# Optimization experiments

Hardware: AMD Instinct MI355X
Metric: run time of the kernel (lower is better)

The kernel has to match this reference:

```python
import jax, jax.numpy as jnp
import numpy as np

N_NODES = 100000
N_EDGES = 1600000
N_GRAPHS = 64
IN_CH = 128
HID = 128
N_CLASSES = 8


def setup_inputs() -> dict:
    key = jax.random.key(0)
    ks = jax.random.split(key, 8)
    x = jax.random.normal(ks[0], (N_NODES, IN_CH), dtype=jnp.float32)
    edge_index = jax.random.randint(ks[1], (2, N_EDGES), 0, N_NODES, dtype=jnp.int64)
    batch = jnp.sort(jax.random.randint(ks[2], (N_NODES,), 0, N_GRAPHS, dtype=jnp.int64))
    s1 = 1.0 / np.sqrt(IN_CH)
    s2 = 1.0 / np.sqrt(HID)
    W1 = jax.random.normal(ks[3], (IN_CH, HID), dtype=jnp.float32) * s1
    b1 = jnp.zeros((HID,), dtype=jnp.float32)
    W2 = jax.random.normal(ks[4], (HID, HID), dtype=jnp.float32) * s2
    b2 = jnp.zeros((HID,), dtype=jnp.float32)
    lin_W = jax.random.normal(ks[5], (HID, N_CLASSES), dtype=jnp.float32) * s2
    lin_b = jnp.zeros((N_CLASSES,), dtype=jnp.float32)
    return {"x": x, "edge_index": edge_index, "batch": batch,
            "W1": W1, "b1": b1, "W2": W2, "b2": b2,
            "lin_W": lin_W, "lin_b": lin_b}


def _gcn_norm(edge_index, n_nodes):
    # add self-loops, compute symmetric normalization coefficients
    loops = jnp.arange(n_nodes, dtype=edge_index.dtype)
    src = jnp.concatenate([edge_index[0], loops])
    dst = jnp.concatenate([edge_index[1], loops])
    ones = jnp.ones(src.shape[0], dtype=jnp.float32)
    deg = jax.ops.segment_sum(ones, dst, num_segments=n_nodes)
    dinv = jnp.where(deg > 0, jax.lax.rsqrt(jnp.maximum(deg, 1.0)), 0.0)
    norm = dinv[src] * dinv[dst]  # [E + N]
    return src, dst, norm


def _gcn_conv(x, W, b, src, dst, norm, n_nodes):
    xw = x @ W                               # [N, H]
    msg = xw[src] * norm[:, None]            # gather + scale, [E+N, H]
    out = jax.ops.segment_sum(msg, dst, num_segments=n_nodes)
    return out + b


def reference(x, edge_index, batch, W1, b1, W2, b2, lin_W, lin_b):
    n = x.shape[0]
    src, dst, norm = _gcn_norm(edge_index, n)
    h = jax.nn.relu(_gcn_conv(x, W1, b1, src, dst, norm, n))
    h = _gcn_conv(h, W2, b2, src, dst, norm, n)
    # global mean pool over graphs
    sums = jax.ops.segment_sum(h, batch, num_segments=N_GRAPHS)
    cnts = jax.ops.segment_sum(jnp.ones(n, dtype=h.dtype), batch, num_segments=N_GRAPHS)
    pooled = sums / jnp.maximum(cnts, 1.0)[:, None]
    return pooled @ lin_W + lin_b
```

## Files before the change

### kernel.cpp

```cpp
#include <hip/hip_runtime.h>
#include <hip/hip_fp16.h>
#include <cstdint>
#include <cstddef>

#define NNODES 100000
#define NEDGES 1600000
#define NGRAPHS 64
#define BSHIFT 7
#define BRANGE 128
#define NB 782
#define CAP 4096
#define NZ NB
#define LP 136
#define NAB 25000

typedef short short8v __attribute__((ext_vector_type(8)));
typedef float float4v __attribute__((ext_vector_type(4)));

__device__ inline short f2h_s(float f) {
    __half h = __float2half(f);
    return __builtin_bit_cast(short, h);
}
__device__ inline ushort f2h_u(float f) {
    __half h = __float2half(f);
    return __builtin_bit_cast(ushort, h);
}
__device__ inline __half2 u2h2(uint u) { return __builtin_bit_cast(__half2, u); }
__device__ inline uint h22u(__half2 h) { return __builtin_bit_cast(uint, h); }


__global__ __launch_bounds__(256) void k_setup(int* __restrict__ zb,
                                               const float* __restrict__ W1,
                                               const float* __restrict__ W2,
                                               short8v* __restrict__ o1,
                                               short8v* __restrict__ o2,
                                               const int* __restrict__ batch,
                                               int* __restrict__ gstart,
                                               int* __restrict__ gend) {
    int b = blockIdx.x, t = threadIdx.x;
    if (b < 4) {
        int i = b * 256 + t;
        if (i < NZ) zb[i] = 0;
    } else if (b < 6) {
        const float* W = (b == 5) ? W2 : W1;
        short8v* o = (b == 5) ? o2 : o1;
        for (int s = t; s < 2048; s += 256) {
            int p = s >> 6, l = s & 63;
            int kb = (p >> 3) * 32 + ((l >> 4) * 8);
            int j = (p & 7) * 16 + (l & 15);
            short8v v;
            #pragma unroll
            for (int i = 0; i < 8; ++i)
                v[i] = f2h_s(W[(size_t)(kb + i) * 128 + j]);
            o[s] = v;
        }
    } else {
        int i = (b - 6) * 256 + t;
        if (i < NNODES) {
            int bb = batch[i];
            if (i == 0 || batch[i - 1] != bb) gstart[bb] = i;
            if (i == NNODES - 1 || batch[i + 1] != bb) gend[bb] = i + 1;
        }
    }
}


#define P1_EPT 16
__global__ __launch_bounds__(256) void k_bscatter(const int* __restrict__ src,
                                                  const int* __restrict__ dst,
                                                  int* __restrict__ bcur,
                                                  uint* __restrict__ pairs, int E) {
    __shared__ int h[NB];
    __shared__ int base[NB];
    int t = threadIdx.x;
    long long c0 = (long long)blockIdx.x * 4096;
    if (c0 >= E) return;
    for (int i = t; i < NB; i += 256) h[i] = 0;
    __syncthreads();
    int myb[P1_EPT], mylp[P1_EPT];
    uint myv[P1_EPT];
    #pragma unroll
    for (int k = 0; k < P1_EPT; ++k) {
        long long e = c0 + t + k * 256;
        if (e < E) {
            int d = dst[e];
            myv[k] = (uint)src[e] | ((uint)(d & (BRANGE - 1)) << 24);
            myb[k] = d >> BSHIFT;
            mylp[k] = atomicAdd(&h[myb[k]], 1);
        } else myb[k] = -1;
    }
    __syncthreads();
    for (int i = t; i < NB; i += 256)
        base[i] = h[i] ? atomicAdd(&bcur[i], h[i]) : 0;
    __syncthreads();
    #pragma unroll
    for (int k = 0; k < P1_EPT; ++k)
        if (myb[k] >= 0) {
            int pos = base[myb[k]] + mylp[k];
            if (pos < CAP)
                pairs[(size_t)myb[k] * CAP + pos] = myv[k];
        }
}


__global__ __launch_bounds__(256) void k_build(const uint* __restrict__ pairs,
                                               const int* __restrict__ bcur,
                                               int2* __restrict__ nr,
                                               float* __restrict__ dinv,
                                               int* __restrict__ csr, int N) {
    __shared__ int h[256];
    __shared__ int sh[256];
    __shared__ int cur[BRANGE];
    int b = blockIdx.x, t = threadIdx.x;
    h[t] = 0;
    __syncthreads();
    const int p0 = b * CAP;
    const int cntb = min(bcur[b], CAP);
    for (int p = t; p < cntb; p += 256)
        atomicAdd(&h[pairs[p0 + p] >> 24], 1);
    __syncthreads();
    int myh = h[t];
    sh[t] = myh;
    __syncthreads();
    #pragma unroll
    for (int d = 1; d < 256; d <<= 1) {
        int val = (t >= d) ? sh[t - d] : 0;
        __syncthreads();
        sh[t] += val;
        __syncthreads();
    }
    int excl = sh[t] - myh;
    int node = (b << BSHIFT) + t;
    if (t < BRANGE) {
        cur[t] = p0 + excl;
        if (node < N) {
            nr[node] = make_int2(p0 + excl, p0 + excl + myh);
            dinv[node] = rsqrtf((float)(myh + 1));
        }
    }
    __syncthreads();
    for (int p = t; p < cntb; p += 256) {
        uint pr = pairs[p0 + p];
        int pos = atomicAdd(&cur[pr >> 24], 1);
        csr[pos] = (int)(pr & 0x00FFFFFFu);
    }
}


__global__ __launch_bounds__(256) void k_gemm_f32(const float* __restrict__ X,
                                                  const short8v* __restrict__ wf,
                                                  const float* __restrict__ dinv,
                                                  ushort* __restrict__ Y, int nrows) {
    __shared__ short8v sW[2048];
    const int tid = threadIdx.x;
    const int lane = tid & 63;
    const int w = tid >> 6;

    for (int s = tid; s < 2048; s += 256) sW[s] = wf[s];
    __syncthreads();

    const int row0 = blockIdx.x * 64 + w * 16;
    const int arow = row0 + (lane & 15);
    float4v acc[8];
    #pragma unroll
    for (int ct = 0; ct < 8; ++ct) acc[ct] = (float4v)0.f;

    #pragma unroll
    for (int kk = 0; kk < 4; ++kk) {
        short8v a = (short8v)0;
        if (arow < nrows) {
            const float* xp = X + (size_t)arow * 128 + kk * 32 + ((lane >> 4) * 8);
            float4 f0 = ((const float4*)xp)[0];
            float4 f1 = ((const float4*)xp)[1];
            a[0] = f2h_s(f0.x); a[1] = f2h_s(f0.y);
            a[2] = f2h_s(f0.z); a[3] = f2h_s(f0.w);
            a[4] = f2h_s(f1.x); a[5] = f2h_s(f1.y);
            a[6] = f2h_s(f1.z); a[7] = f2h_s(f1.w);
        }
        #pragma unroll
        for (int ct = 0; ct < 8; ++ct)
            acc[ct] = __builtin_amdgcn_mfma_f32_16x16x32_f16(a, sW[(kk * 8 + ct) * 64 + lane],
                                                             acc[ct], 0, 0, 0);
    }

    const int orow = row0 + ((lane >> 4) << 2);
    #pragma unroll
    for (int r = 0; r < 4; ++r) {
        int row = orow + r;
        if (row < nrows) {
            float dr = dinv[row];
            #pragma unroll
            for (int ct = 0; ct < 8; ++ct)
                Y[(size_t)row * 128 + ct * 16 + (lane & 15)] = f2h_u(acc[ct][r] * dr);
        }
    }
}


__global__ __launch_bounds__(256, 8) void k_agg_gemm(const uint* __restrict__ msg,
                                                     const float* __restrict__ dinv,
                                                     const int2* __restrict__ nr,
                                                     const int* __restrict__ csr,
                                                     const float* __restrict__ bias,
                                                     const short8v* __restrict__ wf,
                                                     ushort* __restrict__ Y, int n) {
    __shared__ ushort ht[16 * LP];
    const int t = threadIdx.x;
    const int lane = t & 63;
    const int w = t >> 6;
    const int row0 = blockIdx.x * 16;
    const float bx = bias[lane * 2];
    const float by = bias[lane * 2 + 1];

    for (int i = 0; i < 4; ++i) {
        const int r = w * 4 + i;
        const int wid = row0 + r;
        __half2 a0 = u2h2(msg[(size_t)wid * 64 + lane]);
        __half2 a1 = u2h2(0u), a2 = u2h2(0u);
        const int2 rg = nr[wid];
        const int e0 = rg.x, e1 = rg.y;
        for (int e = e0; e < e1; e += 64) {
            int me = e + lane;
            int sidx = (me < e1) ? csr[me] : 0;
            int cnt = min(64, e1 - e);
            for (int kb = 0; kb < cnt; kb += 6) {
                int lim = cnt - 1;
                int s0 = __shfl(sidx, min(kb + 0, lim));
                int s1 = __shfl(sidx, min(kb + 1, lim));
                int s2 = __shfl(sidx, min(kb + 2, lim));
                int s3 = __shfl(sidx, min(kb + 3, lim));
                int s4 = __shfl(sidx, min(kb + 4, lim));
                int s5 = __shfl(sidx, min(kb + 5, lim));
                uint u0 = msg[(size_t)s0 * 64 + lane];
                uint u1 = msg[(size_t)s1 * 64 + lane];
                uint u2 = msg[(size_t)s2 * 64 + lane];
                uint u3 = msg[(size_t)s3 * 64 + lane];
                uint u4 = msg[(size_t)s4 * 64 + lane];
                uint u5 = msg[(size_t)s5 * 64 + lane];
                u1 = (kb + 1 < cnt) ? u1 : 0u;
                u2 = (kb + 2 < cnt) ? u2 : 0u;
                u3 = (kb + 3 < cnt) ? u3 : 0u;
                u4 = (kb + 4 < cnt) ? u4 : 0u;
                u5 = (kb + 5 < cnt) ? u5 : 0u;
                a0 = __hadd2(a0, u2h2(u0));
                a1 = __hadd2(a1, u2h2(u1));
                a2 = __hadd2(a2, u2h2(u2));
                a0 = __hadd2(a0, u2h2(u3));
                a1 = __hadd2(a1, u2h2(u4));
                a2 = __hadd2(a2, u2h2(u5));
            }
        }
        __half2 acc = __hadd2(__hadd2(a0, a1), a2);
        float2 f = __half22float2(acc);
        float dd = dinv[wid];
        float ax = fmaxf(f.x * dd + bx, 0.f);
        float ay = fmaxf(f.y * dd + by, 0.f);
        *(uint*)&ht[r * LP + lane * 2] = h22u(__floats2half2_rn(ax, ay));
    }
    __syncthreads();

    float4v acc[2];
    acc[0] = (float4v)0.f;
    acc[1] = (float4v)0.f;
    const int arow = lane & 15;
    const int ct0 = w * 2;
    #pragma unroll
    for (int kk = 0; kk < 4; ++kk) {
        short8v a = *(const short8v*)&ht[arow * LP + kk * 32 + ((lane >> 4) * 8)];
        acc[0] = __builtin_amdgcn_mfma_f32_16x16x32_f16(a, wf[(kk * 8 + ct0) * 64 + lane],
                                                        acc[0], 0, 0, 0);
        acc[1] = __builtin_amdgcn_mfma_f32_16x16x32_f16(a, wf[(kk * 8 + ct0 + 1) * 64 + lane],
                                                        acc[1], 0, 0, 0);
    }
    const int orow = row0 + ((lane >> 4) << 2);
    #pragma unroll
    for (int r = 0; r < 4; ++r) {
        int row = orow + r;
        float dr = dinv[row];
        Y[(size_t)row * 128 + ct0 * 16 + (lane & 15)]       = f2h_u(acc[0][r] * dr);
        Y[(size_t)row * 128 + (ct0 + 1) * 16 + (lane & 15)] = f2h_u(acc[1][r] * dr);
    }
}


__global__ __launch_bounds__(256) void k_agg_pool(const uint* __restrict__ msg,
                                                  const float* __restrict__ dinv,
                                                  const int2* __restrict__ nr,
                                                  const int* __restrict__ csr,
                                                  const int* __restrict__ batch,
                                                  float* __restrict__ pA,
                                                  float* __restrict__ pB) {
    __shared__ float red[4][128];
    __shared__ int selw[4];
    const int blk = blockIdx.x;
    const int t = threadIdx.x;
    const int lane = t & 63;
    const int w = t >> 6;
    const int wid = blk * 4 + w;

    __half2 a0 = u2h2(msg[(size_t)wid * 64 + lane]);
    __half2 a1 = u2h2(0u), a2 = u2h2(0u);
    const int2 rg = nr[wid];
    const int e0 = rg.x, e1 = rg.y;
    for (int e = e0; e < e1; e += 64) {
        int me = e + lane;
        int sidx = (me < e1) ? csr[me] : 0;
        int cnt = min(64, e1 - e);
        for (int kb = 0; kb < cnt; kb += 6) {
            int lim = cnt - 1;
            int s0 = __shfl(sidx, min(kb + 0, lim));
            int s1 = __shfl(sidx, min(kb + 1, lim));
            int s2 = __shfl(sidx, min(kb + 2, lim));
            int s3 = __shfl(sidx, min(kb + 3, lim));
            int s4 = __shfl(sidx, min(kb + 4, lim));
            int s5 = __shfl(sidx, min(kb + 5, lim));
            uint u0 = msg[(size_t)s0 * 64 + lane];
            uint u1 = msg[(size_t)s1 * 64 + lane];
            uint u2 = msg[(size_t)s2 * 64 + lane];
            uint u3 = msg[(size_t)s3 * 64 + lane];
            uint u4 = msg[(size_t)s4 * 64 + lane];
            uint u5 = msg[(size_t)s5 * 64 + lane];
            u1 = (kb + 1 < cnt) ? u1 : 0u;
            u2 = (kb + 2 < cnt) ? u2 : 0u;
            u3 = (kb + 3 < cnt) ? u3 : 0u;
            u4 = (kb + 4 < cnt) ? u4 : 0u;
            u5 = (kb + 5 < cnt) ? u5 : 0u;
            a0 = __hadd2(a0, u2h2(u0));
            a1 = __hadd2(a1, u2h2(u1));
            a2 = __hadd2(a2, u2h2(u2));
            a0 = __hadd2(a0, u2h2(u3));
            a1 = __hadd2(a1, u2h2(u4));
            a2 = __hadd2(a2, u2h2(u5));
        }
    }
    __half2 acc = __hadd2(__hadd2(a0, a1), a2);
    float2 f = __half22float2(acc);
    float dd = dinv[wid];
    red[w][lane * 2] = f.x * dd;
    red[w][lane * 2 + 1] = f.y * dd;
    if (lane == 0) selw[w] = (batch[wid] != batch[blk * 4]) ? 1 : 0;
    __syncthreads();
    if (t < 128) {
        float a = 0.f, b = 0.f;
        #pragma unroll
        for (int ww = 0; ww < 4; ++ww) {
            float v = red[ww][t];
            if (selw[ww]) b += v; else a += v;
        }
        pA[(size_t)blk * 128 + t] = a;
        if (selw[0] | selw[1] | selw[2] | selw[3])
            pB[(size_t)blk * 128 + t] = b;
    }
}


__global__ __launch_bounds__(512) void k_final(const float* __restrict__ pA,
                                               const float* __restrict__ pB,
                                               const int* __restrict__ batch,
                                               const int* __restrict__ gstart,
                                               const int* __restrict__ gend,
                                               const float* __restrict__ b2,
                                               const float* __restrict__ linW,
                                               const float* __restrict__ linb,
                                               float* __restrict__ out) {
    __shared__ float sq[4][128];
    __shared__ float red[128][8];
    int g = blockIdx.x;
    int t = threadIdx.x;
    int c = t & 127;
    int q = t >> 7;
    int b0 = gstart[g] >> 2;
    int b1 = (gend[g] - 1) >> 2;
    float v = 0.f;
    #pragma unroll 4
    for (int b = b0 + 1 + q; b <= b1; b += 4)
        v += pA[(size_t)b * 128 + c];
    if (q == 0)
        v += ((batch[b0 * 4] != g) ? pB : pA)[(size_t)b0 * 128 + c];
    sq[q][c] = v;
    __syncthreads();
    if (t < 128) {
        float sv = sq[0][t] + sq[1][t] + sq[2][t] + sq[3][t];
        float cnt = (float)(gend[g] - gstart[g]);
        sv = sv / fmaxf(cnt, 1.0f) + b2[t];
        #pragma unroll
        for (int k = 0; k < 8; ++k) red[t][k] = sv * linW[(size_t)t * 8 + k];
    }
    __syncthreads();
    #pragma unroll
    for (int st = 64; st > 0; st >>= 1) {
        if (t < st) {
            #pragma unroll
            for (int k = 0; k < 8; ++k) red[t][k] += red[t + st][k];
        }
        __syncthreads();
    }
    if (t < 8) out[(size_t)g * 8 + t] = red[0][t] + linb[t];
}


extern "C" void kernel_launch(void* const* d_in, const int* in_sizes, int n_in,
                              void* d_out, int out_size, void* d_ws, size_t ws_size,
                              hipStream_t stream) {
    const float* x     = (const float*)d_in[0];
    const int*   ei    = (const int*)d_in[1];
    const int*   batch = (const int*)d_in[2];
    const float* W1    = (const float*)d_in[3];
    const float* b1    = (const float*)d_in[4];
    const float* W2    = (const float*)d_in[5];
    const float* b2    = (const float*)d_in[6];
    const float* linW  = (const float*)d_in[7];
    const float* linb  = (const float*)d_in[8];
    float* out = (float*)d_out;

    const int N = NNODES, E = NEDGES;
    const int* src = ei;
    const int* dst = ei + E;

    char* ws = (char*)d_ws;
    uint*  bufA16 = (uint*)ws;     ws += (size_t)N * 64 * 4;
    uint*  bufH16 = (uint*)ws;     ws += (size_t)N * 64 * 4;
    float* dinv   = (float*)ws;    ws += (size_t)N * 4;
    int2*  nr     = (int2*)ws;     ws += (size_t)N * 8;
    int*   csr    = (int*)ws;      ws += (size_t)NB * CAP * 4;
    int*   bcur   = (int*)ws;      ws += NB * 4;
    int*   gstart = (int*)ws;      ws += NGRAPHS * 4;
    int*   gend   = (int*)ws;      ws += NGRAPHS * 4;
    short8v* wf1  = (short8v*)ws;  ws += 2048 * 16;
    short8v* wf2  = (short8v*)ws;  ws += 2048 * 16;
    float* pA     = (float*)ws;    ws += (size_t)NAB * 128 * 4;
    float* pB     = (float*)ws;    ws += (size_t)NAB * 128 * 4;
    uint*  pairs  = (uint*)bufH16;

    const int B = 256;

    k_setup<<<397, B, 0, stream>>>(bcur, W1, W2, wf1, wf2, batch, gstart, gend);

    k_bscatter<<<(E + 4095) / 4096, B, 0, stream>>>(src, dst, bcur, pairs, E);
    k_build<<<NB, B, 0, stream>>>(pairs, bcur, nr, dinv, csr, N);

    k_gemm_f32<<<(N + 63) / 64, B, 0, stream>>>(x, wf1, dinv, (ushort*)bufA16, N);

    k_agg_gemm<<<N / 16, B, 0, stream>>>(bufA16, dinv, nr, csr, b1, wf2,
                                         (ushort*)bufH16, N);

    k_agg_pool<<<NAB, B, 0, stream>>>(bufH16, dinv, nr, csr, batch, pA, pB);

    k_final<<<NGRAPHS, 512, 0, stream>>>(pA, pB, batch, gstart, gend, b2, linW, linb, out);
}
```

Before: 204.5 us.

## Stage X tiles through LDS in first GEMM and widen aggregation blocks

The first GEMM now handles 16 rows per block. It stages the fp32 rows as fp16 in shared memory with coalesced float4 loads and reads W fragments straight from global memory, so each block no longer copies the full 32KB weight into LDS. The aggregation+GEMM kernel moves to 512 threads, with 8 waves each aggregating 2 rows and computing one 16-column tile. This raises parallelism in the gather phase, at the cost of more blocks each reloading weights from global/L2 and dropping the nrows bounds check (N is divisible by 16).

```diff
diff --git a/kernel.cpp b/kernel.cpp
--- a/kernel.cpp
+++ b/kernel.cpp
@@ -147,63 +147,58 @@
 }
 
 
-__global__ __launch_bounds__(256) void k_gemm_f32(const float* __restrict__ X,
+__global__ __launch_bounds__(256) void k_gemm_f32(const float4* __restrict__ X4,
                                                   const short8v* __restrict__ wf,
                                                   const float* __restrict__ dinv,
-                                                  ushort* __restrict__ Y, int nrows) {
-    __shared__ short8v sW[2048];
-    const int tid = threadIdx.x;
-    const int lane = tid & 63;
-    const int w = tid >> 6;
-
-    for (int s = tid; s < 2048; s += 256) sW[s] = wf[s];
-    __syncthreads();
-
-    const int row0 = blockIdx.x * 64 + w * 16;
-    const int arow = row0 + (lane & 15);
-    float4v acc[8];
-    #pragma unroll
-    for (int ct = 0; ct < 8; ++ct) acc[ct] = (float4v)0.f;
-
+                                                  ushort* __restrict__ Y, int n) {
+    __shared__ ushort ht[16 * LP];
+    const int t = threadIdx.x;
+    const int lane = t & 63;
+    const int w = t >> 6;
+    const int row0 = blockIdx.x * 16;
+
+    #pragma unroll
+    for (int s = t; s < 16 * 32; s += 256) {
+        int row = s >> 5, q = s & 31;
+        float4 v = X4[(size_t)(row0 + row) * 32 + q];
+        ushort2 h0 = make_ushort2(f2h_u(v.x), f2h_u(v.y));
+        ushort2 h1 = make_ushort2(f2h_u(v.z), f2h_u(v.w));
+        *(ushort2*)&ht[row * LP + q * 4] = h0;
+        *(ushort2*)&ht[row * LP + q * 4 + 2] = h1;
+    }
+    __syncthreads();
+
+    float4v acc[2];
+    acc[0] = (float4v)0.f;
+    acc[1] = (float4v)0.f;
+    const int arow = lane & 15;
+    const int ct0 = w * 2;
     #pragma unroll
     for (int kk = 0; kk < 4; ++kk) {
-        short8v a = (short8v)0;
-        if (arow < nrows) {
-            const float* xp = X + (size_t)arow * 128 + kk * 32 + ((lane >> 4) * 8);
-            float4 f0 = ((const float4*)xp)[0];
-            float4 f1 = ((const float4*)xp)[1];
-            a[0] = f2h_s(f0.x); a[1] = f2h_s(f0.y);
-            a[2] = f2h_s(f0.z); a[3] = f2h_s(f0.w);
-            a[4] = f2h_s(f1.x); a[5] = f2h_s(f1.y);
-            a[6] = f2h_s(f1.z); a[7] = f2h_s(f1.w);
-        }
-        #pragma unroll
-        for (int ct = 0; ct < 8; ++ct)
-            acc[ct] = __builtin_amdgcn_mfma_f32_16x16x32_f16(a, sW[(kk * 8 + ct) * 64 + lane],
-                                                             acc[ct], 0, 0, 0);
-    }
-
+        short8v a = *(const short8v*)&ht[arow * LP + kk * 32 + ((lane >> 4) * 8)];
+        acc[0] = __builtin_amdgcn_mfma_f32_16x16x32_f16(a, wf[(kk * 8 + ct0) * 64 + lane],
+                                                        acc[0], 0, 0, 0);
+        acc[1] = __builtin_amdgcn_mfma_f32_16x16x32_f16(a, wf[(kk * 8 + ct0 + 1) * 64 + lane],
+                                                        acc[1], 0, 0, 0);
+    }
     const int orow = row0 + ((lane >> 4) << 2);
     #pragma unroll
     for (int r = 0; r < 4; ++r) {
         int row = orow + r;
-        if (row < nrows) {
-            float dr = dinv[row];
-            #pragma unroll
-            for (int ct = 0; ct < 8; ++ct)
-                Y[(size_t)row * 128 + ct * 16 + (lane & 15)] = f2h_u(acc[ct][r] * dr);
-        }
-    }
-}
-
-
-__global__ __launch_bounds__(256, 8) void k_agg_gemm(const uint* __restrict__ msg,
-                                                     const float* __restrict__ dinv,
-                                                     const int2* __restrict__ nr,
-                                                     const int* __restrict__ csr,
-                                                     const float* __restrict__ bias,
-                                                     const short8v* __restrict__ wf,
-                                                     ushort* __restrict__ Y, int n) {
+        float dr = dinv[row];
+        Y[(size_t)row * 128 + ct0 * 16 + (lane & 15)]       = f2h_u(acc[0][r] * dr);
+        Y[(size_t)row * 128 + (ct0 + 1) * 16 + (lane & 15)] = f2h_u(acc[1][r] * dr);
+    }
+}
+
+
+__global__ __launch_bounds__(512) void k_agg_gemm(const uint* __restrict__ msg,
+                                                  const float* __restrict__ dinv,
+                                                  const int2* __restrict__ nr,
+                                                  const int* __restrict__ csr,
+                                                  const float* __restrict__ bias,
+                                                  const short8v* __restrict__ wf,
+                                                  ushort* __restrict__ Y, int n) {
     __shared__ ushort ht[16 * LP];
     const int t = threadIdx.x;
     const int lane = t & 63;
@@ -212,8 +207,9 @@
     const float bx = bias[lane * 2];
     const float by = bias[lane * 2 + 1];
 
-    for (int i = 0; i < 4; ++i) {
-        const int r = w * 4 + i;
+    #pragma unroll
+    for (int i = 0; i < 2; ++i) {
+        const int r = w * 2 + i;
         const int wid = row0 + r;
         __half2 a0 = u2h2(msg[(size_t)wid * 64 + lane]);
         __half2 a1 = u2h2(0u), a2 = u2h2(0u);
@@ -259,26 +255,20 @@
     }
     __syncthreads();
 
-    float4v acc[2];
-    acc[0] = (float4v)0.f;
-    acc[1] = (float4v)0.f;
+    float4v acc = (float4v)0.f;
     const int arow = lane & 15;
-    const int ct0 = w * 2;
     #pragma unroll
     for (int kk = 0; kk < 4; ++kk) {
         short8v a = *(const short8v*)&ht[arow * LP + kk * 32 + ((lane >> 4) * 8)];
-        acc[0] = __builtin_amdgcn_mfma_f32_16x16x32_f16(a, wf[(kk * 8 + ct0) * 64 + lane],
-                                                        acc[0], 0, 0, 0);
-        acc[1] = __builtin_amdgcn_mfma_f32_16x16x32_f16(a, wf[(kk * 8 + ct0 + 1) * 64 + lane],
-                                                        acc[1], 0, 0, 0);
+        acc = __builtin_amdgcn_mfma_f32_16x16x32_f16(a, wf[(kk * 8 + w) * 64 + lane],
+                                                     acc, 0, 0, 0);
     }
     const int orow = row0 + ((lane >> 4) << 2);
     #pragma unroll
     for (int r = 0; r < 4; ++r) {
         int row = orow + r;
         float dr = dinv[row];
-        Y[(size_t)row * 128 + ct0 * 16 + (lane & 15)]       = f2h_u(acc[0][r] * dr);
-        Y[(size_t)row * 128 + (ct0 + 1) * 16 + (lane & 15)] = f2h_u(acc[1][r] * dr);
+        Y[(size_t)row * 128 + w * 16 + (lane & 15)] = f2h_u(acc[r] * dr);
     }
 }
 
@@ -439,10 +429,10 @@
     k_bscatter<<<(E + 4095) / 4096, B, 0, stream>>>(src, dst, bcur, pairs, E);
     k_build<<<NB, B, 0, stream>>>(pairs, bcur, nr, dinv, csr, N);
 
-    k_gemm_f32<<<(N + 63) / 64, B, 0, stream>>>(x, wf1, dinv, (ushort*)bufA16, N);
-
-    k_agg_gemm<<<N / 16, B, 0, stream>>>(bufA16, dinv, nr, csr, b1, wf2,
-                                         (ushort*)bufH16, N);
+    k_gemm_f32<<<N / 16, B, 0, stream>>>((const float4*)x, wf1, dinv, (ushort*)bufA16, N);
+
+    k_agg_gemm<<<N / 16, 512, 0, stream>>>(bufA16, dinv, nr, csr, b1, wf2,
+                                           (ushort*)bufH16, N);
 
     k_agg_pool<<<NAB, B, 0, stream>>>(bufH16, dinv, nr, csr, batch, pA, pB);
 
```

New measurement: 200.4 us. 2.0% less time.
